# Optimization experiments

Hardware: AMD Instinct MI355X
Metric: run time of the kernel (lower is better)

Reference implementation:

```python
import jax, jax.numpy as jnp
import numpy as np

# Module hyperparameters (from init_kwargs)
IOU_T = 0.5
PROB_T = 0.75
COV = 10.0
TOPK = 500       # self.topk
PRE_K = 2048     # fixed-shape cap on post-threshold candidates entering NMS
B, C, H, W = 4, 4, 160, 160


def setup_inputs() -> dict:
    key = jax.random.key(0)
    k1, k2 = jax.random.split(key)
    mask = jax.random.normal(k1, (B, C, H, W), dtype=jnp.float32)
    # scale bias so boxes have ~10px extent (realistic detections)
    bias = jax.random.normal(k2, (B, 4, H, W), dtype=jnp.float32) * 8.0
    return {"mask": mask, "bias": bias}


def _pos_grid(h, w):
    # equivalent of np.dstack(np.mgrid[0:h, 0:w]) -> [h, w, 2] with (y, x)
    yy, xx = jnp.meshgrid(jnp.arange(h), jnp.arange(w), indexing="ij")
    return jnp.stack([yy, xx], axis=-1).astype(jnp.float32)


def _pairwise_iou(b):
    # b: [K, 4] as (y1, x1, y2, x2); torchvision-style IoU (areas unclamped, inter clamped)
    area = (b[:, 2] - b[:, 0]) * (b[:, 3] - b[:, 1])
    lt = jnp.maximum(b[:, None, :2], b[None, :, :2])
    rb = jnp.minimum(b[:, None, 2:], b[None, :, 2:])
    wh = jnp.clip(rb - lt, 0.0)
    inter = wh[..., 0] * wh[..., 1]
    return inter / (area[:, None] + area[None, :] - inter)


def _nms_keep(iou, valid, thresh):
    # boxes are pre-sorted by descending score; greedy suppression
    K = iou.shape[0]
    idx = jnp.arange(K)
    def body(i, keep):
        sup = (iou[i] > thresh) & (idx > i) & keep[i]
        return keep & ~sup
    return jax.lax.fori_loop(0, K, body, valid)


def _per_image(mask_i, bias_i, pos):
    # mask_i: [C, h, w], bias_i: [4, h, w], pos: [h, w, 2]
    p = jax.nn.softmax(mask_i, axis=0)
    prob = jax.lax.stop_gradient(p.max(axis=0))          # prob.detach()
    cls = p.argmax(axis=0)
    frontal = (cls != 0) & (prob > PROB_T)               # [h, w]
    # boxes = pos tiled to (y,x,y,x) + bias.permute(0,2,3,1)
    boxes = jnp.concatenate([pos, pos], axis=-1) + jnp.transpose(bias_i, (1, 2, 0))
    boxes = boxes.reshape(-1, 4)                          # [h*w, 4]
    score = jnp.where(frontal.reshape(-1), prob.reshape(-1), -1.0)
    # fixed-size candidate set, sorted by descending score (invalid -> -1)
    top_s, idx = jax.lax.top_k(score, PRE_K)
    cand = boxes[idx]
    valid = top_s > 0.0                                   # valid scores > PROB_T > 0
    keep = _nms_keep(_pairwise_iou(cand), valid, IOU_T)
    kept_s = jnp.where(keep, top_s, -1.0)
    fin_s, fi = jax.lax.top_k(kept_s, TOPK)               # min(topk, n) via padding
    fboxes = cand[fi]                                     # [TOPK, 4]
    fvalid = fin_s > 0.0
    fprob = jnp.where(fvalid, fin_s, 0.0)
    mu = (fboxes[:, :2] + fboxes[:, 2:]) * 0.5            # [TOPK, 2]
    sigma = fboxes[:, 2:] - fboxes[:, :2]
    sigma = jnp.where(fvalid[:, None], sigma, 1.0)        # safe divisor for padding
    # gaussian2d: z = (pos - mu) / (sigma / cov); heat = max_n exp(-|z|^2/2) * prob
    z = (pos[None] - mu[:, None, None, :]) / (sigma[:, None, None, :] / COV)  # [TOPK,h,w,2]
    g = jnp.exp(-0.5 * (z ** 2).sum(axis=-1)) * fprob[:, None, None]
    heat = g.max(axis=0)                                  # [h, w]; all-padded -> 0, matches n==0 case
    return heat, fboxes, fvalid


def reference(mask, bias):
    pos = _pos_grid(mask.shape[2], mask.shape[3])
    heat, fboxes, fvalid = jax.vmap(lambda m, b: _per_image(m, b, pos))(mask, bias)
    # original returns (heatmaps, mask, boxes); boxes padded to [B, TOPK, 4] with validity mask
    return heat, mask, fboxes, fvalid
```

## Files before the change

### kernel.cpp

```cpp
#include <hip/hip_runtime.h>
#include <math.h>

#define BATCH 4
#define NCH 4
#define H 160
#define W 160
#define NPIX (H * W)
#define NTILE (NPIX / 256)
#define PRE_K 2048
#define TOPK 500
#define PROB_T 0.75f
#define IOU_T 0.5f
#define COV 10.0f
#define RK_CH 4096

#define FCNT_OFF  0u
#define BCNT_OFF  64u
#define BMASK_OFF 4096u
#define KEY_OFF   20480u
#define CSC_OFF   839680u
#define CBOX_OFF  872448u
#define SUP_OFF   1003520u
#define FLAG_OFF  3100672u

#define OUT_HEAT_OFF 0
#define OUT_MASK_OFF 102400
#define OUT_BOX_OFF  512000
#define OUT_VAL_OFF  520000

#define TILE 16
#define TPL (W / TILE)

typedef unsigned long long u64;
typedef unsigned int u32;

__device__ __forceinline__ int block_scan_excl(int v, int tid, int* tmp, int* total) {
    tmp[tid] = v;
    __syncthreads();
    for (int off = 1; off < 256; off <<= 1) {
        int y = (tid >= off) ? tmp[tid - off] : 0;
        __syncthreads();
        tmp[tid] += y;
        __syncthreads();
    }
    int incl = tmp[tid];
    *total = tmp[255];
    __syncthreads();
    return incl - v;
}

__global__ void __launch_bounds__(256)
k_score(const float* __restrict__ mask, float* __restrict__ out_mask,
        u64* __restrict__ keys, u64* __restrict__ bmask,
        int* __restrict__ blkcnt, int* __restrict__ Fcnt) {
    int b = blockIdx.y, bx = blockIdx.x, tid = threadIdx.x;
    int pix = bx * 256 + tid;
    const float* mp = mask + (size_t)b * NCH * NPIX + pix;
    float* op = out_mask + (size_t)b * NCH * NPIX + pix;
    float x0 = mp[0], x1 = mp[NPIX], x2 = mp[2 * NPIX], x3 = mp[3 * NPIX];
    op[0] = x0; op[NPIX] = x1; op[2 * NPIX] = x2; op[3 * NPIX] = x3;
    float mx = x0; int c = 0;
    if (x1 > mx) { mx = x1; c = 1; }
    if (x2 > mx) { mx = x2; c = 2; }
    if (x3 > mx) { mx = x3; c = 3; }
    float sum = ((expf(x0 - mx) + expf(x1 - mx)) + expf(x2 - mx)) + expf(x3 - mx);
    float prob = 1.0f / sum;
    bool fr = (c != 0) && (prob > PROB_T);

    int lane = tid & 63, wv = tid >> 6;
    u64 bm = __ballot(fr);
    __shared__ int wcnt[4];
    __shared__ int wpre[4];
    __shared__ int base_s;
    if (lane == 0) {
        bmask[(size_t)b * (NPIX / 64) + bx * 4 + wv] = bm;
        wcnt[wv] = __popcll(bm);
    }
    __syncthreads();
    if (tid == 0) {
        int acc = 0;
        #pragma unroll
        for (int k = 0; k < 4; ++k) { wpre[k] = acc; acc += wcnt[k]; }
        blkcnt[b * NTILE + bx] = acc;
        base_s = (acc > 0) ? atomicAdd(&Fcnt[b], acc) : 0;
    }
    __syncthreads();
    if (fr) {
        int slot = base_s + wpre[wv] + __popcll(bm & ((1ull << lane) - 1ull));
        keys[(size_t)b * NPIX + slot] =
            ((u64)__float_as_uint(prob) << 32) | (u64)(0x7FFFFFFFu - (u32)pix);
    }
}

__global__ void __launch_bounds__(256)
k_rank(const u64* __restrict__ keys, const float* __restrict__ bias,
       const int* __restrict__ Fcnt, const int* __restrict__ blkcnt,
       const u64* __restrict__ bmask, float* __restrict__ cand_score,
       float* __restrict__ cand_box) {
    int b = blockIdx.y, bx = blockIdx.x, tid = threadIdx.x;
    int F = Fcnt[b];
    int blk0 = bx * 256;
    if (blk0 >= F && blk0 >= PRE_K) return;
    int i = blk0 + tid;
    const float* bb = bias + (size_t)b * 4 * NPIX;

    __shared__ u64 ks[RK_CH];
    if (blk0 < F) {
        const u64* kb = keys + (size_t)b * NPIX;
        u64 ki = (i < F) ? kb[i] : 0;
        int rank = 0;
        for (int base = 0; base < F; base += RK_CH) {
            int lim = min(RK_CH, F - base);
            __syncthreads();
            for (int k = tid; k < lim; k += 256) ks[k] = kb[base + k];
            __syncthreads();
            if (i < F) {
                int k = 0;
                for (; k + 8 <= lim; k += 8) {
                    rank += (ks[k]     > ki) ? 1 : 0;
                    rank += (ks[k + 1] > ki) ? 1 : 0;
                    rank += (ks[k + 2] > ki) ? 1 : 0;
                    rank += (ks[k + 3] > ki) ? 1 : 0;
                    rank += (ks[k + 4] > ki) ? 1 : 0;
                    rank += (ks[k + 5] > ki) ? 1 : 0;
                    rank += (ks[k + 6] > ki) ? 1 : 0;
                    rank += (ks[k + 7] > ki) ? 1 : 0;
                }
                for (; k < lim; ++k) rank += (ks[k] > ki) ? 1 : 0;
            }
        }
        if (i < F && rank < PRE_K) {
            float si = __uint_as_float((u32)(ki >> 32));
            int xi = 0x7FFFFFFF - (int)(u32)(ki & 0xFFFFFFFFu);
            cand_score[(size_t)b * PRE_K + rank] = si;
            float y = (float)(xi / W), x = (float)(xi % W);
            float4 box;
            box.x = y + bb[0 * NPIX + xi];
            box.y = x + bb[1 * NPIX + xi];
            box.z = y + bb[2 * NPIX + xi];
            box.w = x + bb[3 * NPIX + xi];
            ((float4*)cand_box)[(size_t)b * PRE_K + rank] = box;
        }
    }
    if (i >= F && i < PRE_K) {
        int j = i - F;
        const int* bc = blkcnt + b * NTILE;
        int t = 0;
        for (; t < NTILE; ++t) {
            int nf = 256 - bc[t];
            if (j < nf) break;
            j -= nf;
        }
        const u64* bmk = bmask + (size_t)b * (NPIX / 64) + t * 4;
        int pix = 0;
        #pragma unroll
        for (int w = 0; w < 4; ++w) {
            u64 bm = bmk[w];
            int nz = 64 - __popcll(bm);
            if (j < nz) {
                u64 x = bm;
                for (int q = 0; q < j; ++q) x |= x + 1;
                pix = t * 256 + w * 64 + __builtin_ctzll(~x);
                break;
            }
            j -= nz;
        }
        cand_score[(size_t)b * PRE_K + i] = -1.0f;
        float y = (float)(pix / W), x = (float)(pix % W);
        float4 box;
        box.x = y + bb[0 * NPIX + pix];
        box.y = x + bb[1 * NPIX + pix];
        box.z = y + bb[2 * NPIX + pix];
        box.w = x + bb[3 * NPIX + pix];
        ((float4*)cand_box)[(size_t)b * PRE_K + i] = box;
    }
}

__global__ void __launch_bounds__(512)
k_iou(const float* __restrict__ cand_box, const int* __restrict__ Fcnt,
      u32* __restrict__ sup, unsigned char* __restrict__ flag) {
    int b = blockIdx.y;
    int F = Fcnt[b];
    int V = F < PRE_K ? F : PRE_K;
    int r0 = blockIdx.x * 8;
    if (r0 >= V) return;
    __shared__ float ly1[PRE_K], lx1[PRE_K], ly2[PRE_K], lx2[PRE_K], lar[PRE_K];
    for (int k = threadIdx.x; k < PRE_K; k += 512) {
        float4 v = ((const float4*)cand_box)[(size_t)b * PRE_K + k];
        ly1[k] = v.x; lx1[k] = v.y; ly2[k] = v.z; lx2[k] = v.w;
        lar[k] = (v.z - v.x) * (v.w - v.y);
    }
    __syncthreads();
    int lr = threadIdx.x >> 6;
    int w = threadIdx.x & 63;
    int i = r0 + lr;
    float ay1 = ly1[i], ax1 = lx1[i], ay2 = ly2[i], ax2 = lx2[i], aa = lar[i];
    u32 bits = 0;
    int jbase = w * 32;
    #pragma unroll 4
    for (int jj = 0; jj < 32; ++jj) {
        int jo = (jj + w) & 31;
        int j = jbase + jo;
        if (j > i) {
            float lty = fmaxf(ay1, ly1[j]);
            float ltx = fmaxf(ax1, lx1[j]);
            float rby = fminf(ay2, ly2[j]);
            float rbx = fminf(ax2, lx2[j]);
            float wy = fmaxf(rby - lty, 0.0f);
            float wx = fmaxf(rbx - ltx, 0.0f);
            float inter = wy * wx;
            float iou = inter / ((aa + lar[j]) - inter);
            if (iou > IOU_T) bits |= (1u << jo);
        }
    }
    bool any = __any(bits != 0u);
    if (any) sup[((size_t)b * PRE_K + i) * 64 + w] = bits;
    if (w == 0) flag[(size_t)b * PRE_K + i] = any ? 1 : 0;
}

__global__ void __launch_bounds__(256)
k_nmsheat(const u32* __restrict__ sup, const unsigned char* __restrict__ flag,
          const int* __restrict__ Fcnt, const float* __restrict__ cand_score,
          const float* __restrict__ cand_box, float* __restrict__ out_boxes,
          float* __restrict__ out_valid, float* __restrict__ heat) {
    int b = blockIdx.y, bx = blockIdx.x, tid = threadIdx.x;
    int F = Fcnt[b];
    int V = F < PRE_K ? F : PRE_K;

    __shared__ int rid_s[PRE_K];
    __shared__ int M_s;
    __shared__ u32 kws[64];
    __shared__ int tmp[256];
    __shared__ float plocal[TOPK * 5];
    __shared__ float lp[TOPK * 5];
    __shared__ int cnum;

    if (tid < 64) {
        int lane = tid;
        const u32* f32p = (const u32*)(flag + (size_t)b * PRE_K);
        u32 fw[8];
        #pragma unroll
        for (int k = 0; k < 8; ++k) fw[k] = f32p[lane * 8 + k];
        int r0 = lane * 32;
        int cnt = 0;
        #pragma unroll
        for (int k = 0; k < 8; ++k)
            #pragma unroll
            for (int j = 0; j < 4; ++j) {
                int r = r0 + k * 4 + j;
                if (((fw[k] >> (8 * j)) & 0xFFu) != 0u && r < V) ++cnt;
            }
        int incl = cnt;
        for (int off = 1; off < 64; off <<= 1) {
            int y = __shfl_up(incl, off);
            if (lane >= off) incl += y;
        }
        if (lane == 63) M_s = incl;
        int pos = incl - cnt;
        #pragma unroll
        for (int k = 0; k < 8; ++k)
            #pragma unroll
            for (int j = 0; j < 4; ++j) {
                int r = r0 + k * 4 + j;
                if (((fw[k] >> (8 * j)) & 0xFFu) != 0u && r < V) rid_s[pos++] = r;
            }

        int M = M_s;
        int rem = V - lane * 32;
        u32 kw = (rem >= 32) ? 0xFFFFFFFFu : (rem <= 0 ? 0u : ((1u << rem) - 1u));
        const u32* supb = sup + (size_t)b * PRE_K * 64 + lane;
        int C = (M + 7) >> 3;
        int C4 = (C + 3) & ~3;
        int l7 = lane & 7;
        u32 rbuf[4][8];
        int ridv[4];

        #define LOAD_RID(slot, c) ridv[slot] = rid_s[min((c) * 8 + l7, PRE_K - 1)]
        #define ISSUE(slot) do { \
            _Pragma("unroll") \
            for (int k_ = 0; k_ < 8; ++k_) { \
                int i_ = __builtin_amdgcn_readlane(ridv[slot], k_) & (PRE_K - 1); \
                rbuf[slot][k_] = supb[(size_t)i_ * 64]; \
            } \
        } while (0)
        #define PROC(slot, c) do { \
            _Pragma("unroll") \
            for (int k_ = 0; k_ < 8; ++k_) { \
                int m_ = (c) * 8 + k_; \
                if (m_ < M) { \
                    int i_ = __builtin_amdgcn_readlane(ridv[slot], k_) & (PRE_K - 1); \
                    u32 kb_ = (u32)__builtin_amdgcn_readlane((int)kw, i_ >> 5); \
                    if ((kb_ >> (i_ & 31)) & 1u) kw &= ~rbuf[slot][k_]; \
                } \
            } \
        } while (0)

        LOAD_RID(0, 0); LOAD_RID(1, 1); LOAD_RID(2, 2); LOAD_RID(3, 3);
        ISSUE(0); ISSUE(1); ISSUE(2);
        for (int c = 0; c < C4; c += 4) {
            PROC(0, c);     ISSUE(3);            LOAD_RID(0, c + 4);
            PROC(1, c + 1); ISSUE(0);            LOAD_RID(1, c + 5);
            PROC(2, c + 2); ISSUE(1);            LOAD_RID(2, c + 6);
            PROC(3, c + 3); ISSUE(2);            LOAD_RID(3, c + 7);
        }
        #undef LOAD_RID
        #undef ISSUE
        #undef PROC
        kws[lane] = kw;
    }
    if (tid == 0) cnum = 0;
    __syncthreads();

    bool writer = (bx == 0);
    int s0 = tid * 8;
    int bits8 = (int)((kws[s0 >> 5] >> (s0 & 31)) & 0xFFu);
    int cnt = __popc(bits8);
    int tot;
    int kpre = block_scan_excl(cnt, tid, tmp, &tot);
    int NK = tot;
    for (int k = 0; k < 8; ++k) {
        int s = s0 + k;
        int kept = (bits8 >> k) & 1;
        int pos = kept ? kpre : (NK + s - kpre);
        if (pos < TOPK) {
            if (kept) {
                float4 bb4 = ((const float4*)cand_box)[(size_t)b * PRE_K + s];
                float scv = cand_score[(size_t)b * PRE_K + s];
                float* q = plocal + pos * 5;
                q[0] = (bb4.x + bb4.z) * 0.5f;
                q[1] = (bb4.y + bb4.w) * 0.5f;
                q[2] = COV / (bb4.z - bb4.x);
                q[3] = COV / (bb4.w - bb4.y);
                q[4] = scv;
                if (writer) {
                    ((float4*)out_boxes)[(size_t)b * TOPK + pos] = bb4;
                    out_valid[(size_t)b * TOPK + pos] = 1.0f;
                }
            } else if (writer) {
                float4 bb4 = ((const float4*)cand_box)[(size_t)b * PRE_K + s];
                ((float4*)out_boxes)[(size_t)b * TOPK + pos] = bb4;
                out_valid[(size_t)b * TOPK + pos] = 0.0f;
            }
        }
        kpre += kept;
    }
    __syncthreads();

    int nv = NK < TOPK ? NK : TOPK;
    int ty0 = (bx / TPL) * TILE;
    int tx0 = (bx % TPL) * TILE;
    for (int t = tid; t < nv; t += 256) {
        const float* pp = plocal + t * 5;
        float muy = pp[0], mux = pp[1], ivy = pp[2], ivx = pp[3], p = pp[4];
        float cy = fmaxf(fmaxf((float)ty0 - muy, muy - (float)(ty0 + TILE - 1)), 0.0f);
        float cx = fmaxf(fmaxf((float)tx0 - mux, mux - (float)(tx0 + TILE - 1)), 0.0f);
        float zy = cy * fabsf(ivy);
        float zx = cx * fabsf(ivx);
        float z2 = zy * zy + zx * zx;
        if (!(z2 > 40.0f)) {
            int idx = atomicAdd(&cnum, 1);
            float* q = lp + idx * 5;
            q[0] = muy; q[1] = mux; q[2] = ivy; q[3] = ivx; q[4] = p;
        }
    }
    __syncthreads();
    int n = cnum;
    float py = (float)(ty0 + (tid >> 4));
    float px = (float)(tx0 + (tid & 15));
    float m = 0.0f;
    for (int t = 0; t < n; ++t) {
        float muy = lp[t * 5 + 0], mux = lp[t * 5 + 1];
        float ivy = lp[t * 5 + 2], ivx = lp[t * 5 + 3];
        float p = lp[t * 5 + 4];
        float zy = (py - muy) * ivy;
        float zx = (px - mux) * ivx;
        float g = expf(-0.5f * (zy * zy + zx * zx)) * p;
        m = fmaxf(m, g);
    }
    heat[(size_t)b * NPIX + (ty0 + (tid >> 4)) * W + tx0 + (tid & 15)] = m;
}

extern "C" void kernel_launch(void* const* d_in, const int* in_sizes, int n_in,
                              void* d_out, int out_size, void* d_ws, size_t ws_size,
                              hipStream_t stream) {
    const float* mask = (const float*)d_in[0];
    const float* bias = (const float*)d_in[1];
    float* out = (float*)d_out;
    char* ws = (char*)d_ws;

    int*   Fcnt       = (int*)(ws + FCNT_OFF);
    int*   blkcnt     = (int*)(ws + BCNT_OFF);
    u64*   bmask      = (u64*)(ws + BMASK_OFF);
    u64*   keys       = (u64*)(ws + KEY_OFF);
    float* cand_score = (float*)(ws + CSC_OFF);
    float* cand_box   = (float*)(ws + CBOX_OFF);
    u32*   sup        = (u32*)(ws + SUP_OFF);
    unsigned char* flag = (unsigned char*)(ws + FLAG_OFF);

    hipMemsetAsync(Fcnt, 0, BATCH * sizeof(int), stream);
    dim3 g100(NTILE, BATCH);
    k_score<<<g100, 256, 0, stream>>>(mask, out + OUT_MASK_OFF, keys, bmask,
                                      blkcnt, Fcnt);
    k_rank<<<g100, 256, 0, stream>>>(keys, bias, Fcnt, blkcnt, bmask,
                                     cand_score, cand_box);
    k_iou<<<dim3(PRE_K / 8, BATCH), 512, 0, stream>>>(cand_box, Fcnt, sup, flag);
    k_nmsheat<<<g100, 256, 0, stream>>>(sup, flag, Fcnt, cand_score, cand_box,
                                        out + OUT_BOX_OFF, out + OUT_VAL_OFF,
                                        out + OUT_HEAT_OFF);
}
```

Measured before the change: 111.8 us.

## Fuse scoring and ranking into one kernel with shared-memory candidate list

Merges the scoring and rank-by-count kernels into a single kernel and drops the memset that cleared the global counter. Each of 12 blocks per image recomputes the full softmax and threshold pass serially over all tiles. This builds the compacted key list and validity bitmask in shared memory, so no global keys, block counts or atomics are needed. It removes a launch, a memset and a global round trip, at the cost of redundant per-block work and a serial tile loop with two barriers per tile. Candidate handling is capped at 4096 in shared memory and 3072 by thread coverage, which would break if more pixels pass the threshold.

New measurement: 186.1 us. 1.66x slower.

```diff
diff --git a/kernel.cpp b/kernel.cpp
--- a/kernel.cpp
+++ b/kernel.cpp
@@ -7,21 +7,21 @@
 #define W 160
 #define NPIX (H * W)
 #define NTILE (NPIX / 256)
+#define NWORD (NPIX / 64)
 #define PRE_K 2048
 #define TOPK 500
 #define PROB_T 0.75f
 #define IOU_T 0.5f
 #define COV 10.0f
-#define RK_CH 4096
-
-#define FCNT_OFF  0u
-#define BCNT_OFF  64u
-#define BMASK_OFF 4096u
-#define KEY_OFF   20480u
-#define CSC_OFF   839680u
-#define CBOX_OFF  872448u
-#define SUP_OFF   1003520u
-#define FLAG_OFF  3100672u
+
+#define KA_BLOCKS 12
+#define KLIST_CAP 4096
+
+#define F_OFF     0u
+#define CSC_OFF   64u
+#define CBOX_OFF  32832u
+#define SUP_OFF   163904u
+#define FLAG_OFF  2261056u
 
 #define OUT_HEAT_OFF 0
 #define OUT_MASK_OFF 102400
@@ -50,86 +50,78 @@
 }
 
 __global__ void __launch_bounds__(256)
-k_score(const float* __restrict__ mask, float* __restrict__ out_mask,
-        u64* __restrict__ keys, u64* __restrict__ bmask,
-        int* __restrict__ blkcnt, int* __restrict__ Fcnt) {
+kA(const float* __restrict__ mask, const float* __restrict__ bias,
+   float* __restrict__ out_mask, int* __restrict__ Fout,
+   float* __restrict__ cand_score, float* __restrict__ cand_box) {
     int b = blockIdx.y, bx = blockIdx.x, tid = threadIdx.x;
-    int pix = bx * 256 + tid;
-    const float* mp = mask + (size_t)b * NCH * NPIX + pix;
-    float* op = out_mask + (size_t)b * NCH * NPIX + pix;
-    float x0 = mp[0], x1 = mp[NPIX], x2 = mp[2 * NPIX], x3 = mp[3 * NPIX];
-    op[0] = x0; op[NPIX] = x1; op[2 * NPIX] = x2; op[3 * NPIX] = x3;
-    float mx = x0; int c = 0;
-    if (x1 > mx) { mx = x1; c = 1; }
-    if (x2 > mx) { mx = x2; c = 2; }
-    if (x3 > mx) { mx = x3; c = 3; }
-    float sum = ((expf(x0 - mx) + expf(x1 - mx)) + expf(x2 - mx)) + expf(x3 - mx);
-    float prob = 1.0f / sum;
-    bool fr = (c != 0) && (prob > PROB_T);
-
     int lane = tid & 63, wv = tid >> 6;
-    u64 bm = __ballot(fr);
+    __shared__ u64 klist[KLIST_CAP];
+    __shared__ u64 bmask[NWORD];
     __shared__ int wcnt[4];
-    __shared__ int wpre[4];
-    __shared__ int base_s;
-    if (lane == 0) {
-        bmask[(size_t)b * (NPIX / 64) + bx * 4 + wv] = bm;
-        wcnt[wv] = __popcll(bm);
-    }
-    __syncthreads();
-    if (tid == 0) {
-        int acc = 0;
+    __shared__ int run_s;
+    if (tid == 0) run_s = 0;
+    __syncthreads();
+
+    const float* mp = mask + (size_t)b * NCH * NPIX;
+    float* op = out_mask + (size_t)b * NCH * NPIX;
+    for (int it = 0; it < NTILE; ++it) {
+        int pix = it * 256 + tid;
+        float x0 = mp[pix], x1 = mp[NPIX + pix];
+        float x2 = mp[2 * NPIX + pix], x3 = mp[3 * NPIX + pix];
+        if (it % KA_BLOCKS == bx) {
+            op[pix] = x0; op[NPIX + pix] = x1;
+            op[2 * NPIX + pix] = x2; op[3 * NPIX + pix] = x3;
+        }
+        float mx = x0; int c = 0;
+        if (x1 > mx) { mx = x1; c = 1; }
+        if (x2 > mx) { mx = x2; c = 2; }
+        if (x3 > mx) { mx = x3; c = 3; }
+        float sum = ((expf(x0 - mx) + expf(x1 - mx)) + expf(x2 - mx)) + expf(x3 - mx);
+        float prob = 1.0f / sum;
+        bool fr = (c != 0) && (prob > PROB_T);
+        u64 bm = __ballot(fr);
+        if (lane == 0) {
+            bmask[it * 4 + wv] = bm;
+            wcnt[wv] = __popcll(bm);
+        }
+        __syncthreads();
+        int base = run_s;
+        int pre = 0;
         #pragma unroll
-        for (int k = 0; k < 4; ++k) { wpre[k] = acc; acc += wcnt[k]; }
-        blkcnt[b * NTILE + bx] = acc;
-        base_s = (acc > 0) ? atomicAdd(&Fcnt[b], acc) : 0;
-    }
-    __syncthreads();
-    if (fr) {
-        int slot = base_s + wpre[wv] + __popcll(bm & ((1ull << lane) - 1ull));
-        keys[(size_t)b * NPIX + slot] =
-            ((u64)__float_as_uint(prob) << 32) | (u64)(0x7FFFFFFFu - (u32)pix);
-    }
-}
-
-__global__ void __launch_bounds__(256)
-k_rank(const u64* __restrict__ keys, const float* __restrict__ bias,
-       const int* __restrict__ Fcnt, const int* __restrict__ blkcnt,
-       const u64* __restrict__ bmask, float* __restrict__ cand_score,
-       float* __restrict__ cand_box) {
-    int b = blockIdx.y, bx = blockIdx.x, tid = threadIdx.x;
-    int F = Fcnt[b];
-    int blk0 = bx * 256;
-    if (blk0 >= F && blk0 >= PRE_K) return;
-    int i = blk0 + tid;
+        for (int k = 0; k < 3; ++k) if (k < wv) pre += wcnt[k];
+        if (fr) {
+            int slot = base + pre + __popcll(bm & ((1ull << lane) - 1ull));
+            if (slot < KLIST_CAP)
+                klist[slot] = ((u64)__float_as_uint(prob) << 32)
+                            | (u64)(0x7FFFFFFFu - (u32)pix);
+        }
+        __syncthreads();
+        if (tid == 0) run_s += wcnt[0] + wcnt[1] + wcnt[2] + wcnt[3];
+    }
+    __syncthreads();
+    int F = run_s;
+    if (tid == 0 && bx == 0) Fout[b] = F;
+
     const float* bb = bias + (size_t)b * 4 * NPIX;
-
-    __shared__ u64 ks[RK_CH];
-    if (blk0 < F) {
-        const u64* kb = keys + (size_t)b * NPIX;
-        u64 ki = (i < F) ? kb[i] : 0;
+    int i = bx * 256 + tid;
+    int FX = F < KLIST_CAP ? F : KLIST_CAP;
+
+    if (i < FX) {
+        u64 ki = klist[i];
         int rank = 0;
-        for (int base = 0; base < F; base += RK_CH) {
-            int lim = min(RK_CH, F - base);
-            __syncthreads();
-            for (int k = tid; k < lim; k += 256) ks[k] = kb[base + k];
-            __syncthreads();
-            if (i < F) {
-                int k = 0;
-                for (; k + 8 <= lim; k += 8) {
-                    rank += (ks[k]     > ki) ? 1 : 0;
-                    rank += (ks[k + 1] > ki) ? 1 : 0;
-                    rank += (ks[k + 2] > ki) ? 1 : 0;
-                    rank += (ks[k + 3] > ki) ? 1 : 0;
-                    rank += (ks[k + 4] > ki) ? 1 : 0;
-                    rank += (ks[k + 5] > ki) ? 1 : 0;
-                    rank += (ks[k + 6] > ki) ? 1 : 0;
-                    rank += (ks[k + 7] > ki) ? 1 : 0;
-                }
-                for (; k < lim; ++k) rank += (ks[k] > ki) ? 1 : 0;
-            }
-        }
-        if (i < F && rank < PRE_K) {
+        int k = 0;
+        for (; k + 8 <= FX; k += 8) {
+            rank += (klist[k]     > ki) ? 1 : 0;
+            rank += (klist[k + 1] > ki) ? 1 : 0;
+            rank += (klist[k + 2] > ki) ? 1 : 0;
+            rank += (klist[k + 3] > ki) ? 1 : 0;
+            rank += (klist[k + 4] > ki) ? 1 : 0;
+            rank += (klist[k + 5] > ki) ? 1 : 0;
+            rank += (klist[k + 6] > ki) ? 1 : 0;
+            rank += (klist[k + 7] > ki) ? 1 : 0;
+        }
+        for (; k < FX; ++k) rank += (klist[k] > ki) ? 1 : 0;
+        if (rank < PRE_K) {
             float si = __uint_as_float((u32)(ki >> 32));
             int xi = 0x7FFFFFFF - (int)(u32)(ki & 0xFFFFFFFFu);
             cand_score[(size_t)b * PRE_K + rank] = si;
@@ -141,26 +133,16 @@
             box.w = x + bb[3 * NPIX + xi];
             ((float4*)cand_box)[(size_t)b * PRE_K + rank] = box;
         }
-    }
-    if (i >= F && i < PRE_K) {
+    } else if (i >= F && i < PRE_K) {
         int j = i - F;
-        const int* bc = blkcnt + b * NTILE;
-        int t = 0;
-        for (; t < NTILE; ++t) {
-            int nf = 256 - bc[t];
-            if (j < nf) break;
-            j -= nf;
-        }
-        const u64* bmk = bmask + (size_t)b * (NPIX / 64) + t * 4;
         int pix = 0;
-        #pragma unroll
-        for (int w = 0; w < 4; ++w) {
-            u64 bm = bmk[w];
+        for (int w = 0; w < NWORD; ++w) {
+            u64 bm = bmask[w];
             int nz = 64 - __popcll(bm);
             if (j < nz) {
                 u64 x = bm;
                 for (int q = 0; q < j; ++q) x |= x + 1;
-                pix = t * 256 + w * 64 + __builtin_ctzll(~x);
+                pix = w * 64 + __builtin_ctzll(~x);
                 break;
             }
             j -= nz;
@@ -177,10 +159,10 @@
 }
 
 __global__ void __launch_bounds__(512)
-k_iou(const float* __restrict__ cand_box, const int* __restrict__ Fcnt,
-      u32* __restrict__ sup, unsigned char* __restrict__ flag) {
+kB(const float* __restrict__ cand_box, const int* __restrict__ Fout,
+   u32* __restrict__ sup, unsigned char* __restrict__ flag) {
     int b = blockIdx.y;
-    int F = Fcnt[b];
+    int F = Fout[b];
     int V = F < PRE_K ? F : PRE_K;
     int r0 = blockIdx.x * 8;
     if (r0 >= V) return;
@@ -219,12 +201,12 @@
 }
 
 __global__ void __launch_bounds__(256)
-k_nmsheat(const u32* __restrict__ sup, const unsigned char* __restrict__ flag,
-          const int* __restrict__ Fcnt, const float* __restrict__ cand_score,
-          const float* __restrict__ cand_box, float* __restrict__ out_boxes,
-          float* __restrict__ out_valid, float* __restrict__ heat) {
+kC(const u32* __restrict__ sup, const unsigned char* __restrict__ flag,
+   const int* __restrict__ Fout, const float* __restrict__ cand_score,
+   const float* __restrict__ cand_box, float* __restrict__ out_boxes,
+   float* __restrict__ out_valid, float* __restrict__ heat) {
     int b = blockIdx.y, bx = blockIdx.x, tid = threadIdx.x;
-    int F = Fcnt[b];
+    int F = Fout[b];
     int V = F < PRE_K ? F : PRE_K;
 
     __shared__ int rid_s[PRE_K];
@@ -388,23 +370,16 @@
     float* out = (float*)d_out;
     char* ws = (char*)d_ws;
 
-    int*   Fcnt       = (int*)(ws + FCNT_OFF);
-    int*   blkcnt     = (int*)(ws + BCNT_OFF);
-    u64*   bmask      = (u64*)(ws + BMASK_OFF);
-    u64*   keys       = (u64*)(ws + KEY_OFF);
+    int*   Fout       = (int*)(ws + F_OFF);
     float* cand_score = (float*)(ws + CSC_OFF);
     float* cand_box   = (float*)(ws + CBOX_OFF);
     u32*   sup        = (u32*)(ws + SUP_OFF);
     unsigned char* flag = (unsigned char*)(ws + FLAG_OFF);
 
-    hipMemsetAsync(Fcnt, 0, BATCH * sizeof(int), stream);
-    dim3 g100(NTILE, BATCH);
-    k_score<<<g100, 256, 0, stream>>>(mask, out + OUT_MASK_OFF, keys, bmask,
-                                      blkcnt, Fcnt);
-    k_rank<<<g100, 256, 0, stream>>>(keys, bias, Fcnt, blkcnt, bmask,
-                                     cand_score, cand_box);
-    k_iou<<<dim3(PRE_K / 8, BATCH), 512, 0, stream>>>(cand_box, Fcnt, sup, flag);
-    k_nmsheat<<<g100, 256, 0, stream>>>(sup, flag, Fcnt, cand_score, cand_box,
-                                        out + OUT_BOX_OFF, out + OUT_VAL_OFF,
-                                        out + OUT_HEAT_OFF);
-}
+    kA<<<dim3(KA_BLOCKS, BATCH), 256, 0, stream>>>(mask, bias, out + OUT_MASK_OFF,
+                                                   Fout, cand_score, cand_box);
+    kB<<<dim3(PRE_K / 8, BATCH), 512, 0, stream>>>(cand_box, Fout, sup, flag);
+    kC<<<dim3(NTILE, BATCH), 256, 0, stream>>>(sup, flag, Fout, cand_score, cand_box,
+                                               out + OUT_BOX_OFF, out + OUT_VAL_OFF,
+                                               out + OUT_HEAT_OFF);
+}
```
